# Optimization experiments

Hardware: AMD Instinct MI355X
Metric: run time of the kernel (lower is better)

The kernel has to match this reference:

```python
import jax, jax.numpy as jnp
import numpy as np

N = 64            # HiPPO order
DT = 1.0 / 512.0  # discretization timestep ~ 1/seq_len


def _hippo_legt_discrete(n, dt):
    """Continuous HiPPO-LegT (A,B) then bilinear (Tustin) discretization,
    matching scipy.signal.cont2discrete(..., method='bilinear')."""
    Q = np.arange(n, dtype=np.float64)
    R = (2 * Q + 1)[:, None]
    j, i = np.meshgrid(Q, Q)
    A = np.where(i < j, -1.0, (-1.0) ** (i - j + 1)) * R
    B = (-1.0) ** Q[:, None] * R  # (n, 1)
    I = np.eye(n)
    ima = I - (dt / 2.0) * A
    Ad = np.linalg.solve(ima, I + (dt / 2.0) * A)
    Bd = np.linalg.solve(ima, dt * B).squeeze(-1)  # (n,)
    return Ad, Bd


def setup_inputs() -> dict:
    key = jax.random.key(0)
    inputs = jax.random.normal(key, (16, 128, 512), dtype=jnp.float32)  # (b, d, L)
    Ad, Bd = _hippo_legt_discrete(N, DT)
    return {
        "inputs": inputs,
        "A": jnp.asarray(Ad, dtype=jnp.float32),  # (N, N)
        "B": jnp.asarray(Bd, dtype=jnp.float32),  # (N,)
    }


def reference(inputs, A, B):
    # inputs: (b, d, L) -> iterate over last axis, state c: (b, d, N)
    fs = jnp.moveaxis(inputs, -1, 0)  # (L, b, d)
    c0 = jnp.zeros(inputs.shape[:-1] + (A.shape[0],), dtype=inputs.dtype)

    def step(c, f):
        # c_t = c_{t-1} @ A^T + f_t[..., None] * B   (F.linear(c, A) == c @ A^T)
        c_new = c @ A.T + f[..., None] * B
        return c_new, c_new

    _, cs = jax.lax.scan(step, c0, fs)
    return cs  # (L, b, d, N)
```

## Files before the change

### kernel.cpp

```cpp
#include <hip/hip_runtime.h>


typedef _Float16 half8  __attribute__((ext_vector_type(8)));
typedef float    f32x4  __attribute__((ext_vector_type(4)));

#define SEQN 2048
#define LT   512

typedef const __attribute__((address_space(1))) unsigned int kGU32;
typedef __attribute__((address_space(3))) unsigned int kLU32;

__device__ __forceinline__ void cp16(const void* g, void* l) {
  __builtin_amdgcn_global_load_lds((kGU32*)g, (kLU32*)l, 16, 0, 0);
}

__device__ __forceinline__ void mul64(const float* XT, const float* Y,
                                      float* outT, float* outN, int t) {
  const int r = (t >> 5) * 4;
  const int c = (t & 31) * 2;
  float a00 = 0.f, a01 = 0.f, a10 = 0.f, a11 = 0.f;
  float a20 = 0.f, a21 = 0.f, a30 = 0.f, a31 = 0.f;
#pragma unroll 4
  for (int l = 0; l < 64; ++l) {
    const float4 x = *(const float4*)(XT + l * 64 + r);
    const float2 y = *(const float2*)(Y + l * 64 + c);
    a00 += x.x * y.x; a01 += x.x * y.y;
    a10 += x.y * y.x; a11 += x.y * y.y;
    a20 += x.z * y.x; a21 += x.z * y.y;
    a30 += x.w * y.x; a31 += x.w * y.y;
  }
  __syncthreads();
  if (outT) {
    outT[(c + 0) * 64 + r + 0] = a00; outT[(c + 1) * 64 + r + 0] = a01;
    outT[(c + 0) * 64 + r + 1] = a10; outT[(c + 1) * 64 + r + 1] = a11;
    outT[(c + 0) * 64 + r + 2] = a20; outT[(c + 1) * 64 + r + 2] = a21;
    outT[(c + 0) * 64 + r + 3] = a30; outT[(c + 1) * 64 + r + 3] = a31;
  }
  if (outN) {
    outN[(r + 0) * 64 + c + 0] = a00; outN[(r + 0) * 64 + c + 1] = a01;
    outN[(r + 1) * 64 + c + 0] = a10; outN[(r + 1) * 64 + c + 1] = a11;
    outN[(r + 2) * 64 + c + 0] = a20; outN[(r + 2) * 64 + c + 1] = a21;
    outN[(r + 3) * 64 + c + 0] = a30; outN[(r + 3) * 64 + c + 1] = a31;
  }
  __syncthreads();
}

__global__ __launch_bounds__(512) void squares_fh(
    const float* __restrict__ A, const float* __restrict__ f,
    float* __restrict__ SqT, _Float16* __restrict__ fh) {
  __shared__ float S[4096];
  __shared__ float STr[4096];
  const int t = threadIdx.x;
  if (blockIdx.x == 0) {
    for (int i = t; i < 4096; i += 512) {
      const float v = A[i];
      S[i] = v;
      STr[(i & 63) * 64 + (i >> 6)] = v;
    }
    __syncthreads();
    for (int i = t; i < 4096; i += 512) SqT[i] = STr[i];
    for (int k = 1; k < 9; ++k) {
      mul64(STr, S, STr, S, t);
      for (int i = t; i < 4096; i += 512) SqT[k * 4096 + i] = STr[i];
    }
  } else {
    const size_t g = (size_t)(blockIdx.x - 1) * 512 + t;
    const float4* s = (const float4*)(f + g * 8);
    const float4 a = s[0], b = s[1];
    half8 v;
    v[0] = (_Float16)a.x; v[1] = (_Float16)a.y;
    v[2] = (_Float16)a.z; v[3] = (_Float16)a.w;
    v[4] = (_Float16)b.x; v[5] = (_Float16)b.y;
    v[6] = (_Float16)b.z; v[7] = (_Float16)b.w;
    *(half8*)(fh + g * 8) = v;
  }
}

__global__ __launch_bounds__(512) void kvec_fill(
    const float* __restrict__ SqT, const float* __restrict__ B,
    _Float16* __restrict__ Lc) {
  __shared__ float Kb[8][64];
  const int t = threadIdx.x;
  const int b = blockIdx.x;

  {
    const int ch = b * 512 + t;
    const int c = ch >> 12, n = (ch >> 6) & 63, zc = ch & 63;
    const uint4 zz = {0u, 0u, 0u, 0u};
    *(uint4*)(Lc + (size_t)c * 65536 + n * 1024 + 512 + zc * 8) = zz;
  }
  if (b == 0) {
    for (int e = t; e < 1792; e += 512) {
      int e2 = e, c = 1;
      while (e2 >= 64 * c) { e2 -= 64 * c; ++c; }
      const int n = e2 & 63, dz = e2 >> 6;
      Lc[(size_t)c * 65536 + n * 1024 + (512 - c + dz)] = (_Float16)0.f;
    }
  }

  const int g = t >> 6, n = t & 63;
  const int i = b * 8 + g;
  float kreg = B[n];
  for (int k = 0; k < 9; ++k) {
    Kb[g][n] = kreg;
    __syncthreads();
    if ((i >> k) & 1) {
      const float* Sk = SqT + k * 4096 + n;
      float s = 0.f;
#pragma unroll 16
      for (int m = 0; m < 64; ++m) s += Sk[m * 64] * Kb[g][m];
      kreg = s;
    }
    __syncthreads();
  }
#pragma unroll
  for (int c = 0; c < 8; ++c) {
    const int z = 511 - i - c;
    if (z >= 0) Lc[(size_t)c * 65536 + n * 1024 + z] = (_Float16)kreg;
  }
}

__global__ __launch_bounds__(256) void causal_gemm(
    const _Float16* __restrict__ fh, const _Float16* __restrict__ Lc,
    float* __restrict__ out) {
  __shared__ _Float16 Xs[128 * 64];
  __shared__ _Float16 Ws[128 * 64];

  const int tid = threadIdx.x;
  const int bn = 255 - (int)blockIdx.x;
  const int bm = blockIdx.y;
  const int lane = tid & 63, wid = tid >> 6;
  const int wm = wid >> 1, wn = wid & 1;
  const int l15 = lane & 15, quad = lane >> 4;
  const int KH = (2 * bn + 65) >> 6;

  const int srow = lane >> 3;
  const int jp = (lane & 7) ^ srow;
  const _Float16* xbase =
      fh + (size_t)(bm * 128 + wid * 32 + srow) * LT + jp * 8;

  f32x4 acc[4][4];
  const f32x4 z4 = {0.f, 0.f, 0.f, 0.f};
#pragma unroll
  for (int i = 0; i < 4; ++i)
#pragma unroll
    for (int j = 0; j < 4; ++j) acc[i][j] = z4;

  for (int kh = 0; kh < KH; ++kh) {
    if (kh) __syncthreads();
#pragma unroll
    for (int q = 0; q < 4; ++q) {
      const int rl = wid * 32 + q * 8 + srow;
      cp16(xbase + (size_t)q * 8 * LT + kh * 64, Xs + (wid * 32 + q * 8) * 64);
      const int tau = 2 * bn + (rl >> 6);
      const int n = rl & 63;
      const int o = 511 - tau + kh * 64;
      const int c = o & 7;
      cp16(Lc + (size_t)c * 65536 + n * 1024 + (o - c) + jp * 8,
           Ws + (wid * 32 + q * 8) * 64);
    }
    __syncthreads();

#pragma unroll
    for (int kk = 0; kk < 2; ++kk) {
      half8 av[4], bv[4];
#pragma unroll
      for (int fm = 0; fm < 4; ++fm) {
        const int r = wm * 64 + fm * 16 + l15;
        av[fm] =
            *(const half8*)&Xs[r * 64 + (((kk * 4 + quad) ^ (l15 & 7)) << 3)];
      }
#pragma unroll
      for (int fn = 0; fn < 4; ++fn) {
        const int r = wn * 64 + fn * 16 + l15;
        bv[fn] =
            *(const half8*)&Ws[r * 64 + (((kk * 4 + quad) ^ (l15 & 7)) << 3)];
      }
#pragma unroll
      for (int fm = 0; fm < 4; ++fm)
#pragma unroll
        for (int fn = 0; fn < 4; ++fn)
          acc[fm][fn] = __builtin_amdgcn_mfma_f32_16x16x32_f16(
              av[fm], bv[fn], acc[fm][fn], 0, 0, 0);
    }
  }

  const int taug = bn * 2 + wn;
#pragma unroll
  for (int fm = 0; fm < 4; ++fm) {
#pragma unroll
    for (int rr = 0; rr < 4; ++rr) {
      const size_t row =
          (size_t)taug * SEQN + (bm * 128 + wm * 64 + fm * 16 + quad * 4 + rr);
      float* o = out + row * 64 + l15;
#pragma unroll
      for (int fn = 0; fn < 4; ++fn) o[fn * 16] = acc[fm][fn][rr];
    }
  }
}

extern "C" void kernel_launch(void* const* d_in, const int* in_sizes, int n_in,
                              void* d_out, int out_size, void* d_ws,
                              size_t ws_size, hipStream_t stream) {
  const float* f = (const float*)d_in[0];
  const float* A = (const float*)d_in[1];
  const float* B = (const float*)d_in[2];
  float* out = (float*)d_out;

  _Float16* Lc = (_Float16*)d_ws;
  float* SqT = (float*)((char*)d_ws + (1 << 20));
  _Float16* fh =
      (_Float16*)((char*)d_ws + (1 << 20) + (192 << 10));

  squares_fh<<<257, 512, 0, stream>>>(A, f, SqT, fh);
  kvec_fill<<<64, 512, 0, stream>>>(SqT, B, Lc);
  causal_gemm<<<dim3(256, 16), 256, 0, stream>>>(fh, Lc, out);
}
```

Baseline: 310.7 us.

## Double-buffer LDS tiles in causal GEMM to overlap loads with MFMA

Adds a second LDS buffer for the X and W tiles so the global-to-LDS copies for the next K slice are issued before the current slice's MFMAs run. One barrier per iteration replaces two. Per-thread global addresses are precomputed once instead of recomputed each iteration. LDS use doubles to 64 KB per block, which can lower occupancy. Correctness relies on the barrier waiting for the async global_load_lds copies to finish.

```diff
diff --git a/kernel.cpp b/kernel.cpp
--- a/kernel.cpp
+++ b/kernel.cpp
@@ -123,8 +123,8 @@
 __global__ __launch_bounds__(256) void causal_gemm(
     const _Float16* __restrict__ fh, const _Float16* __restrict__ Lc,
     float* __restrict__ out) {
-  __shared__ _Float16 Xs[128 * 64];
-  __shared__ _Float16 Ws[128 * 64];
+  __shared__ _Float16 Xs[2][128 * 64];
+  __shared__ _Float16 Ws[2][128 * 64];
 
   const int tid = threadIdx.x;
   const int bn = 255 - (int)blockIdx.x;
@@ -136,8 +136,21 @@
 
   const int srow = lane >> 3;
   const int jp = (lane & 7) ^ srow;
-  const _Float16* xbase =
-      fh + (size_t)(bm * 128 + wid * 32 + srow) * LT + jp * 8;
+
+  const _Float16* xp[4];
+  const _Float16* wp[4];
+  int ldso[4];
+#pragma unroll
+  for (int q = 0; q < 4; ++q) {
+    const int rl = wid * 32 + q * 8 + srow;
+    xp[q] = fh + (size_t)(bm * 128 + rl) * LT + jp * 8;
+    const int tau = 2 * bn + (rl >> 6);
+    const int n = rl & 63;
+    const int o0 = 511 - tau;
+    const int c = o0 & 7;
+    wp[q] = Lc + (size_t)c * 65536 + n * 1024 + (o0 - c) + jp * 8;
+    ldso[q] = (wid * 32 + q * 8) * 64;
+  }
 
   f32x4 acc[4][4];
   const f32x4 z4 = {0.f, 0.f, 0.f, 0.f};
@@ -146,20 +159,24 @@
 #pragma unroll
     for (int j = 0; j < 4; ++j) acc[i][j] = z4;
 
+#pragma unroll
+  for (int q = 0; q < 4; ++q) {
+    cp16(xp[q], &Xs[0][ldso[q]]);
+    cp16(wp[q], &Ws[0][ldso[q]]);
+  }
+  __syncthreads();
+
+  int cur = 0;
   for (int kh = 0; kh < KH; ++kh) {
-    if (kh) __syncthreads();
-#pragma unroll
-    for (int q = 0; q < 4; ++q) {
-      const int rl = wid * 32 + q * 8 + srow;
-      cp16(xbase + (size_t)q * 8 * LT + kh * 64, Xs + (wid * 32 + q * 8) * 64);
-      const int tau = 2 * bn + (rl >> 6);
-      const int n = rl & 63;
-      const int o = 511 - tau + kh * 64;
-      const int c = o & 7;
-      cp16(Lc + (size_t)c * 65536 + n * 1024 + (o - c) + jp * 8,
-           Ws + (wid * 32 + q * 8) * 64);
-    }
-    __syncthreads();
+    if (kh + 1 < KH) {
+      const int nxt = cur ^ 1;
+      const size_t go = (size_t)(kh + 1) * 64;
+#pragma unroll
+      for (int q = 0; q < 4; ++q) {
+        cp16(xp[q] + go, &Xs[nxt][ldso[q]]);
+        cp16(wp[q] + go, &Ws[nxt][ldso[q]]);
+      }
+    }
 
 #pragma unroll
     for (int kk = 0; kk < 2; ++kk) {
@@ -167,14 +184,14 @@
 #pragma unroll
       for (int fm = 0; fm < 4; ++fm) {
         const int r = wm * 64 + fm * 16 + l15;
-        av[fm] =
-            *(const half8*)&Xs[r * 64 + (((kk * 4 + quad) ^ (l15 & 7)) << 3)];
+        av[fm] = *(const half8*)&Xs[cur][r * 64 +
+                                         (((kk * 4 + quad) ^ (l15 & 7)) << 3)];
       }
 #pragma unroll
       for (int fn = 0; fn < 4; ++fn) {
         const int r = wn * 64 + fn * 16 + l15;
-        bv[fn] =
-            *(const half8*)&Ws[r * 64 + (((kk * 4 + quad) ^ (l15 & 7)) << 3)];
+        bv[fn] = *(const half8*)&Ws[cur][r * 64 +
+                                         (((kk * 4 + quad) ^ (l15 & 7)) << 3)];
       }
 #pragma unroll
       for (int fm = 0; fm < 4; ++fm)
@@ -183,6 +200,9 @@
           acc[fm][fn] = __builtin_amdgcn_mfma_f32_16x16x32_f16(
               av[fm], bv[fn], acc[fm][fn], 0, 0, 0);
     }
+
+    if (kh + 1 < KH) __syncthreads();
+    cur ^= 1;
   }
 
   const int taug = bn * 2 + wn;
```

New measurement: 316.9 us. About the same (+2.0%).

## Load MFMA operands directly from global memory with register double buffering

Applied to the files above, without the earlier changes.

The causal GEMM no longer stages X and W tiles through LDS with global_load_lds and barriers. Each wave now loads its half8 fragments straight from global memory into registers and double-buffers them across K steps of 32, with a finer K trip count (KQ instead of KH). This removes LDS traffic and block-wide synchronisation, at the cost of uncoalesced 16-byte global loads, redundant loads across waves sharing rows, and more register pressure.

```diff
diff --git a/kernel.cpp b/kernel.cpp
--- a/kernel.cpp
+++ b/kernel.cpp
@@ -6,13 +6,6 @@
 
 #define SEQN 2048
 #define LT   512
-
-typedef const __attribute__((address_space(1))) unsigned int kGU32;
-typedef __attribute__((address_space(3))) unsigned int kLU32;
-
-__device__ __forceinline__ void cp16(const void* g, void* l) {
-  __builtin_amdgcn_global_load_lds((kGU32*)g, (kLU32*)l, 16, 0, 0);
-}
 
 __device__ __forceinline__ void mul64(const float* XT, const float* Y,
                                       float* outT, float* outN, int t) {
@@ -123,21 +116,22 @@
 __global__ __launch_bounds__(256) void causal_gemm(
     const _Float16* __restrict__ fh, const _Float16* __restrict__ Lc,
     float* __restrict__ out) {
-  __shared__ _Float16 Xs[128 * 64];
-  __shared__ _Float16 Ws[128 * 64];
-
   const int tid = threadIdx.x;
   const int bn = 255 - (int)blockIdx.x;
   const int bm = blockIdx.y;
   const int lane = tid & 63, wid = tid >> 6;
   const int wm = wid >> 1, wn = wid & 1;
   const int l15 = lane & 15, quad = lane >> 4;
-  const int KH = (2 * bn + 65) >> 6;
-
-  const int srow = lane >> 3;
-  const int jp = (lane & 7) ^ srow;
-  const _Float16* xbase =
-      fh + (size_t)(bm * 128 + wid * 32 + srow) * LT + jp * 8;
+  const int KQ = (2 * bn + 33) >> 5;
+
+  const int tau = 2 * bn + wn;
+  const int o0 = 511 - tau;
+  const int c = o0 & 7;
+
+  const _Float16* px =
+      fh + (size_t)(bm * 128 + wm * 64 + l15) * LT + quad * 8;
+  const _Float16* pw =
+      Lc + (size_t)c * 65536 + l15 * 1024 + (o0 - c) + quad * 8;
 
   f32x4 acc[4][4];
   const f32x4 z4 = {0.f, 0.f, 0.f, 0.f};
@@ -146,52 +140,43 @@
 #pragma unroll
     for (int j = 0; j < 4; ++j) acc[i][j] = z4;
 
-  for (int kh = 0; kh < KH; ++kh) {
-    if (kh) __syncthreads();
-#pragma unroll
-    for (int q = 0; q < 4; ++q) {
-      const int rl = wid * 32 + q * 8 + srow;
-      cp16(xbase + (size_t)q * 8 * LT + kh * 64, Xs + (wid * 32 + q * 8) * 64);
-      const int tau = 2 * bn + (rl >> 6);
-      const int n = rl & 63;
-      const int o = 511 - tau + kh * 64;
-      const int c = o & 7;
-      cp16(Lc + (size_t)c * 65536 + n * 1024 + (o - c) + jp * 8,
-           Ws + (wid * 32 + q * 8) * 64);
-    }
-    __syncthreads();
-
-#pragma unroll
-    for (int kk = 0; kk < 2; ++kk) {
-      half8 av[4], bv[4];
-#pragma unroll
-      for (int fm = 0; fm < 4; ++fm) {
-        const int r = wm * 64 + fm * 16 + l15;
-        av[fm] =
-            *(const half8*)&Xs[r * 64 + (((kk * 4 + quad) ^ (l15 & 7)) << 3)];
-      }
-#pragma unroll
-      for (int fn = 0; fn < 4; ++fn) {
-        const int r = wn * 64 + fn * 16 + l15;
-        bv[fn] =
-            *(const half8*)&Ws[r * 64 + (((kk * 4 + quad) ^ (l15 & 7)) << 3)];
-      }
-#pragma unroll
-      for (int fm = 0; fm < 4; ++fm)
-#pragma unroll
-        for (int fn = 0; fn < 4; ++fn)
-          acc[fm][fn] = __builtin_amdgcn_mfma_f32_16x16x32_f16(
-              av[fm], bv[fn], acc[fm][fn], 0, 0, 0);
-    }
-  }
-
-  const int taug = bn * 2 + wn;
+#define LOADS(AV, BV, kq)                                          \
+  do {                                                             \
+    const int ko_ = (kq) * 32;                                     \
+    _Pragma("unroll") for (int fm_ = 0; fm_ < 4; ++fm_)            \
+        AV[fm_] = *(const half8*)(px + fm_ * (16 * LT) + ko_);     \
+    _Pragma("unroll") for (int fn_ = 0; fn_ < 4; ++fn_)            \
+        BV[fn_] = *(const half8*)(pw + fn_ * (16 * 1024) + ko_);   \
+  } while (0)
+
+#define MFMAS(AV, BV)                                              \
+  do {                                                             \
+    _Pragma("unroll") for (int fm_ = 0; fm_ < 4; ++fm_)            \
+        _Pragma("unroll") for (int fn_ = 0; fn_ < 4; ++fn_)        \
+            acc[fm_][fn_] = __builtin_amdgcn_mfma_f32_16x16x32_f16(\
+                AV[fm_], BV[fn_], acc[fm_][fn_], 0, 0, 0);         \
+  } while (0)
+
+  half8 aA[4], bA[4], aB[4], bB[4];
+  LOADS(aA, bA, 0);
+  int kq = 0;
+  for (;;) {
+    if (kq + 1 < KQ) LOADS(aB, bB, kq + 1);
+    MFMAS(aA, bA);
+    if (++kq >= KQ) break;
+    if (kq + 1 < KQ) LOADS(aA, bA, kq + 1);
+    MFMAS(aB, bB);
+    if (++kq >= KQ) break;
+  }
+#undef LOADS
+#undef MFMAS
+
 #pragma unroll
   for (int fm = 0; fm < 4; ++fm) {
 #pragma unroll
     for (int rr = 0; rr < 4; ++rr) {
       const size_t row =
-          (size_t)taug * SEQN + (bm * 128 + wm * 64 + fm * 16 + quad * 4 + rr);
+          (size_t)tau * SEQN + (bm * 128 + wm * 64 + fm * 16 + quad * 4 + rr);
       float* o = out + row * 64 + l15;
 #pragma unroll
       for (int fn = 0; fn < 4; ++fn) o[fn * 16] = acc[fm][fn][rr];
```

New measurement: 406.6 us. 1.31x slower.
